# Kernel tuning notes

Measured on AMD Instinct MI355X. Metric: run time of the kernel, lower is better.

The kernel has to match this reference:

```python
import jax, jax.numpy as jnp
import numpy as np
import math

NUM_HEADS = 8
EMBED = 512
D_K = EMBED // NUM_HEADS
B, T1, T2 = 16, 512, 512
N_POS = 2 * T1 - 1


def rel_shift(x, left_context=0):
    # x: (B, H, T1, 2*T1-1) -> (B, H, T1, T2), out[i, j] = x[i, j - i + T1 - 1]
    t1 = x.shape[2]
    t2 = t1 + left_context
    idx = jnp.arange(t2)[None, :] - jnp.arange(t1)[:, None] + (t1 - 1)  # (T1, T2)
    return jnp.take_along_axis(x, idx[None, None, :, :], axis=-1)


def setup_inputs() -> dict:
    key = jax.random.key(0)
    ks = jax.random.split(key, 16)
    scale = 1.0 / math.sqrt(EMBED)
    inp = {
        "query": jax.random.normal(ks[0], (B, T1, EMBED), jnp.float32),
        "key": jax.random.normal(ks[1], (B, T2, EMBED), jnp.float32),
        "value": jax.random.normal(ks[2], (B, T2, EMBED), jnp.float32),
        "pos_enc": jax.random.normal(ks[3], (B, N_POS, EMBED), jnp.float32),
        "mask": jnp.zeros((B, T2), dtype=bool),
        "chunk_mask": jnp.zeros((T1, T1), dtype=bool),
        "Wq": jax.random.normal(ks[4], (EMBED, EMBED), jnp.float32) * scale,
        "bq": jnp.zeros((EMBED,), jnp.float32),
        "Wk": jax.random.normal(ks[5], (EMBED, EMBED), jnp.float32) * scale,
        "bk": jnp.zeros((EMBED,), jnp.float32),
        "Wv": jax.random.normal(ks[6], (EMBED, EMBED), jnp.float32) * scale,
        "bv": jnp.zeros((EMBED,), jnp.float32),
        "Wpos": jax.random.normal(ks[7], (EMBED, EMBED), jnp.float32) * scale,
        "Wo": jax.random.normal(ks[8], (EMBED, EMBED), jnp.float32) * scale,
        "bo": jnp.zeros((EMBED,), jnp.float32),
        "pos_bias_u": jax.random.normal(ks[9], (NUM_HEADS, D_K), jnp.float32) * 0.1,
        "pos_bias_v": jax.random.normal(ks[10], (NUM_HEADS, D_K), jnp.float32) * 0.1,
        "left_context": 0,
    }
    return inp


def reference(query, key, value, pos_enc, mask, chunk_mask, Wq, bq, Wk, bk, Wv, bv,
              Wpos, Wo, bo, pos_bias_u, pos_bias_v, left_context):
    b, t1, _ = query.shape
    t2 = key.shape[1]
    # qkv projections -> (B, T, H, d_k)
    q = (query @ Wq.T + bq).reshape(b, t1, NUM_HEADS, D_K)
    k = (key @ Wk.T + bk).reshape(b, t2, NUM_HEADS, D_K)
    v = (value @ Wv.T + bv).reshape(b, t2, NUM_HEADS, D_K)
    # positional projection (no bias) -> (B, N, H, d_k)
    p = (pos_enc @ Wpos.T).reshape(b, -1, NUM_HEADS, D_K)
    # content and positional scores
    matrix_ac = jnp.einsum('bihd,bjhd->bhij', q + pos_bias_u, k)  # (B,H,T1,T2)
    matrix_bd = jnp.einsum('bihd,bnhd->bhin', q + pos_bias_v, p)  # (B,H,T1,N)
    matrix_bd = rel_shift(matrix_bd, left_context=left_context)   # (B,H,T1,T2)
    scores = (matrix_ac + matrix_bd) / math.sqrt(D_K)
    # combined mask: True = masked
    m = chunk_mask[None, None, :, :] | mask[:, None, None, :]
    neg_inf = jnp.finfo(scores.dtype).min
    scores = jnp.where(m, neg_inf, scores)
    attn = jax.nn.softmax(scores, axis=-1)
    attn = jnp.where(m, 0.0, attn)
    out = jnp.einsum('bhij,bjhd->bihd', attn, v).reshape(b, t1, NUM_HEADS * D_K)
    return out @ Wo.T + bo
```

## Files before the change

kernel.cpp:

```cpp
#include <hip/hip_runtime.h>
#include <math.h>

typedef _Float16 f16;
typedef f16 f16x8 __attribute__((ext_vector_type(8)));
typedef f16 f16x4 __attribute__((ext_vector_type(4)));
typedef float f32x4 __attribute__((ext_vector_type(4)));

#define H_   8
#define E_   512
#define DK   64
#define BB   16
#define T1C  512
#define T2C  512
#define NPOS 1023

__device__ __forceinline__ f16x8 cvt8(const float4 a, const float4 b) {
    f16x8 h;
    h[0] = (f16)a.x; h[1] = (f16)a.y; h[2] = (f16)a.z; h[3] = (f16)a.w;
    h[4] = (f16)b.x; h[5] = (f16)b.y; h[6] = (f16)b.z; h[7] = (f16)b.w;
    return h;
}

struct PArg {
    const void* A; const float* W; const float* bias; const float* bias2;
    void* C; int Mvalid; int mode; int a16;
};
struct PArgs { PArg g[4]; };

__device__ __forceinline__ void gemm64_body(const PArg g, int bx, int by) {
    __shared__ f16 Al[64 * 40];
    __shared__ f16 Wl[64 * 40];
    const int tid = threadIdx.x;
    const int lane = tid & 63, w = tid >> 6;
    const int quad = lane >> 4, l15 = lane & 15;
    const int m0 = by * 64, n0 = bx * 64;
    const int row = tid >> 2, koff = (tid & 3) * 8;
    int arow = m0 + row; if (arow >= g.Mvalid) arow = g.Mvalid - 1;
    const size_t aoff = (size_t)arow * 512 + koff;
    const size_t woff = (size_t)(n0 + row) * 512 + koff;

    f32x4 acc[4];
    #pragma unroll
    for (int nt = 0; nt < 4; ++nt) acc[nt] = (f32x4){0.f, 0.f, 0.f, 0.f};

    float4 fa0, fa1, fw0, fw1;
    uint4 ha;
    if (g.a16) {
        ha = *(const uint4*)((const f16*)g.A + aoff);
    } else {
        fa0 = *(const float4*)((const float*)g.A + aoff);
        fa1 = *(const float4*)((const float*)g.A + aoff + 4);
    }
    fw0 = *(const float4*)(g.W + woff);
    fw1 = *(const float4*)(g.W + woff + 4);

    for (int ki = 0; ki < 16; ++ki) {
        __syncthreads();
        if (g.a16) *(uint4*)&Al[row * 40 + koff] = ha;
        else       *(f16x8*)&Al[row * 40 + koff] = cvt8(fa0, fa1);
        *(f16x8*)&Wl[row * 40 + koff] = cvt8(fw0, fw1);
        __syncthreads();
        if (ki < 15) {
            const int k0 = (ki + 1) * 32;
            if (g.a16) {
                ha = *(const uint4*)((const f16*)g.A + aoff + k0);
            } else {
                fa0 = *(const float4*)((const float*)g.A + aoff + k0);
                fa1 = *(const float4*)((const float*)g.A + aoff + k0 + 4);
            }
            fw0 = *(const float4*)(g.W + woff + k0);
            fw1 = *(const float4*)(g.W + woff + k0 + 4);
        }
        const f16x8 af = *(const f16x8*)&Al[(w * 16 + l15) * 40 + quad * 8];
        #pragma unroll
        for (int nt = 0; nt < 4; ++nt) {
            const f16x8 bf = *(const f16x8*)&Wl[(nt * 16 + l15) * 40 + quad * 8];
            acc[nt] = __builtin_amdgcn_mfma_f32_16x16x32_f16(af, bf, acc[nt], 0, 0, 0);
        }
    }

    const int mb = m0 + w * 16 + quad * 4;
    #pragma unroll
    for (int nt = 0; nt < 4; ++nt) {
        const int n = n0 + nt * 16 + l15;
        const f32x4 a = acc[nt];
        float bs = g.bias ? g.bias[n] : 0.f;
        if (g.bias2) bs += g.bias2[n];
        if (g.mode == 0) {
            float* C = (float*)g.C;
            #pragma unroll
            for (int r = 0; r < 4; ++r) C[(size_t)(mb + r) * 512 + n] = a[r] + bs;
        } else if (g.mode == 1) {
            f16* C = (f16*)g.C;
            const int b = mb >> 9, t = mb & 511;
            const int hh = n >> 6, dk = n & 63;
            f16x4 h;
            #pragma unroll
            for (int r = 0; r < 4; ++r) h[r] = (f16)(a[r] + bs);
            *(f16x4*)&C[(((size_t)b * H_ + hh) * DK + dk) * 512 + t] = h;
        } else if (g.mode == 2) {
            f16* C = (f16*)g.C;
            const int b = mb >> 9, t = mb & 511;
            const int hh = n >> 6, dk = n & 63;
            #pragma unroll
            for (int r = 0; r < 4; ++r)
                C[(((size_t)b * H_ + hh) * 512 + t + r) * DK + dk] = (f16)(a[r] + bs);
        } else {
            f16* C = (f16*)g.C;
            const int hh = n >> 6, dk = n & 63;
            #pragma unroll
            for (int r = 0; r < 4; ++r) {
                const int m = mb + r;
                if (m < g.Mvalid) {
                    const int b = m / NPOS, t = m - b * NPOS;
                    C[(((size_t)b * H_ + hh) * NPOS + t) * DK + dk] = (f16)a[r];
                }
            }
        }
    }
}

__device__ __forceinline__ int xcd_swz(int rem, int nwg) {
    return (rem & 7) * (nwg >> 3) + (rem >> 3);
}

__global__ __launch_bounds__(256) void proj_all(PArgs a) {
    const int id = blockIdx.x;
    int gi, rem, nwg;
    if (id < 3072) { gi = id >> 10; rem = id & 1023; nwg = 1024; }
    else           { gi = 3;        rem = id - 3072; nwg = 2048; }
    const int t = xcd_swz(rem, nwg);
    gemm64_body(a.g[gi], t & 7, t >> 3);
}
__global__ __launch_bounds__(256) void proj_one(PArg g) {
    const int t = xcd_swz(blockIdx.x, 1024);
    gemm64_body(g, t & 7, t >> 3);
}

__global__ __launch_bounds__(256) void attn_mfma(
    const f16* __restrict__ Qh,
    const f16* __restrict__ Kh,
    const f16* __restrict__ Vt,
    const f16* __restrict__ Ph,
    const float* __restrict__ pbu, const float* __restrict__ pbv,
    const unsigned char* __restrict__ bmask,
    const unsigned char* __restrict__ cmask,
    f16* __restrict__ CTX)
{
    __shared__ f16 Qa[64 * 72];
    __shared__ f16 Ka[64 * 72];
    __shared__ f16 Va[64 * 72];
    __shared__ f16 Pa[128 * 72];
    __shared__ unsigned char Ma[64 * 64];

    const int tid = threadIdx.x;
    const int lane = tid & 63, w = tid >> 6;
    const int quad = lane >> 4, l15 = lane & 15;
    const int id = blockIdx.x;
    const int lg = (id & 7) * 128 + (id >> 3);
    const int it = lg & 7, bh = lg >> 3;
    const int h = bh & 7, b = bh >> 3;
    const int i0 = it * 64;
    const int rowt = w * 16 + quad * 4;
    const int sr = tid >> 3, sc = (tid & 7) * 8;
    const int mr = tid >> 2, mc = (tid & 3) * 16;

    *(uint4*)&Qa[sr * 72 + sc] = *(const uint4*)&Qh[((size_t)bh * 512 + i0 + sr) * 64 + sc];
    *(uint4*)&Qa[(sr + 32) * 72 + sc] =
        *(const uint4*)&Qh[((size_t)bh * 512 + i0 + sr + 32) * 64 + sc];
    f16x8 dpbf[2];
    #pragma unroll
    for (int ks = 0; ks < 2; ++ks)
        #pragma unroll
        for (int j = 0; j < 8; ++j) {
            const int d = ks * 32 + quad * 8 + j;
            dpbf[ks][j] = (f16)(pbv[h * 64 + d] - pbu[h * 64 + d]);
        }

    float m_run[4], l_run[4];
    f32x4 accO[4];
    #pragma unroll
    for (int x = 0; x < 4; ++x) {
        m_run[x] = -__builtin_inff(); l_run[x] = 0.f;
        accO[x] = (f32x4){0.f, 0.f, 0.f, 0.f};
    }

    uint4 pK0, pK1, pV0, pV1, pP0, pP1, pP2, pP3, pM;
    {
        const int j0 = 0, nbase = 448 - i0;
        pK0 = *(const uint4*)&Kh[((size_t)bh * 512 + j0 + sr) * 64 + sc];
        pK1 = *(const uint4*)&Kh[((size_t)bh * 512 + j0 + sr + 32) * 64 + sc];
        pV0 = *(const uint4*)&Vt[((size_t)bh * 64 + sr) * 512 + j0 + sc];
        pV1 = *(const uint4*)&Vt[((size_t)bh * 64 + sr + 32) * 512 + j0 + sc];
        int n0_ = nbase + sr;       if (n0_ > NPOS - 1) n0_ = NPOS - 1;
        int n1_ = nbase + sr + 32;  if (n1_ > NPOS - 1) n1_ = NPOS - 1;
        int n2_ = nbase + sr + 64;  if (n2_ > NPOS - 1) n2_ = NPOS - 1;
        int n3_ = nbase + sr + 96;  if (n3_ > NPOS - 1) n3_ = NPOS - 1;
        pP0 = *(const uint4*)&Ph[((size_t)bh * NPOS + n0_) * 64 + sc];
        pP1 = *(const uint4*)&Ph[((size_t)bh * NPOS + n1_) * 64 + sc];
        pP2 = *(const uint4*)&Ph[((size_t)bh * NPOS + n2_) * 64 + sc];
        pP3 = *(const uint4*)&Ph[((size_t)bh * NPOS + n3_) * 64 + sc];
        const uint4 cm = *(const uint4*)&cmask[(size_t)(i0 + mr) * 512 + j0 + mc];
        const uint4 bm = *(const uint4*)&bmask[(size_t)b * 512 + j0 + mc];
        pM.x = cm.x | bm.x; pM.y = cm.y | bm.y; pM.z = cm.z | bm.z; pM.w = cm.w | bm.w;
    }

    for (int jt = 0; jt < 8; ++jt) {
        __syncthreads();
        *(uint4*)&Ka[sr * 72 + sc] = pK0;
        *(uint4*)&Ka[(sr + 32) * 72 + sc] = pK1;
        *(uint4*)&Va[sr * 72 + sc] = pV0;
        *(uint4*)&Va[(sr + 32) * 72 + sc] = pV1;
        *(uint4*)&Pa[sr * 72 + sc] = pP0;
        *(uint4*)&Pa[(sr + 32) * 72 + sc] = pP1;
        *(uint4*)&Pa[(sr + 64) * 72 + sc] = pP2;
        *(uint4*)&Pa[(sr + 96) * 72 + sc] = pP3;
        *(uint4*)&Ma[mr * 64 + mc] = pM;
        __syncthreads();

        if (jt < 7) {
            const int j0n = (jt + 1) * 64;
            const int nbase = j0n - i0 + 448;
            pK0 = *(const uint4*)&Kh[((size_t)bh * 512 + j0n + sr) * 64 + sc];
            pK1 = *(const uint4*)&Kh[((size_t)bh * 512 + j0n + sr + 32) * 64 + sc];
            pV0 = *(const uint4*)&Vt[((size_t)bh * 64 + sr) * 512 + j0n + sc];
            pV1 = *(const uint4*)&Vt[((size_t)bh * 64 + sr + 32) * 512 + j0n + sc];
            int n0_ = nbase + sr;       if (n0_ > NPOS - 1) n0_ = NPOS - 1;
            int n1_ = nbase + sr + 32;  if (n1_ > NPOS - 1) n1_ = NPOS - 1;
            int n2_ = nbase + sr + 64;  if (n2_ > NPOS - 1) n2_ = NPOS - 1;
            int n3_ = nbase + sr + 96;  if (n3_ > NPOS - 1) n3_ = NPOS - 1;
            pP0 = *(const uint4*)&Ph[((size_t)bh * NPOS + n0_) * 64 + sc];
            pP1 = *(const uint4*)&Ph[((size_t)bh * NPOS + n1_) * 64 + sc];
            pP2 = *(const uint4*)&Ph[((size_t)bh * NPOS + n2_) * 64 + sc];
            pP3 = *(const uint4*)&Ph[((size_t)bh * NPOS + n3_) * 64 + sc];
            const uint4 cm = *(const uint4*)&cmask[(size_t)(i0 + mr) * 512 + j0n + mc];
            const uint4 bm = *(const uint4*)&bmask[(size_t)b * 512 + j0n + mc];
            pM.x = cm.x | bm.x; pM.y = cm.y | bm.y; pM.z = cm.z | bm.z; pM.w = cm.w | bm.w;
        }

        f16x8 afQ[2], afV[2];
        #pragma unroll
        for (int ks = 0; ks < 2; ++ks) {
            afQ[ks] = *(const f16x8*)&Qa[(w * 16 + l15) * 72 + ks * 32 + quad * 8];
            afV[ks] = afQ[ks] + dpbf[ks];
        }
        f32x4 accAC[4];
        #pragma unroll
        for (int nt = 0; nt < 4; ++nt) {
            accAC[nt] = (f32x4){0.f, 0.f, 0.f, 0.f};
            #pragma unroll
            for (int ks = 0; ks < 2; ++ks) {
                const f16x8 bf = *(const f16x8*)&Ka[(nt * 16 + l15) * 72 + ks * 32 + quad * 8];
                accAC[nt] = __builtin_amdgcn_mfma_f32_16x16x32_f16(afQ[ks], bf, accAC[nt], 0, 0, 0);
            }
        }
        f32x4 accBD[5];
        #pragma unroll
        for (int u = 0; u < 5; ++u) {
            accBD[u] = (f32x4){0.f, 0.f, 0.f, 0.f};
            const int nts = (3 - w) + u;
            #pragma unroll
            for (int ks = 0; ks < 2; ++ks) {
                const f16x8 bf = *(const f16x8*)&Pa[(nts * 16 + l15) * 72 + ks * 32 + quad * 8];
                accBD[u] = __builtin_amdgcn_mfma_f32_16x16x32_f16(afV[ks], bf, accBD[u], 0, 0, 0);
            }
        }
        __syncthreads();

        #pragma unroll
        for (int rg = 0; rg < 4; ++rg) {
            const int qr = quad * 4 + rg;
            const int rt = rowt + rg;
            float tmpv[5];
            #pragma unroll
            for (int u = 0; u < 5; ++u) {
                const int cl = l15 + (3 + u) * 16 + qr - 63;
                const int dst = (quad * 16 + (cl & 15)) << 2;
                tmpv[u] = __uint_as_float(
                    (unsigned)__builtin_amdgcn_ds_permute(dst, (int)__float_as_uint(accBD[u][rg])));
            }
            const bool hi = l15 > qr;
            float sv[4]; unsigned mk = 0;
            #pragma unroll
            for (int nt = 0; nt < 4; ++nt) {
                const int c = nt * 16 + l15;
                const float bdv = hi ? tmpv[nt + 1] : tmpv[nt];
                float s = (accAC[nt][rg] + bdv) * 0.125f;
                if (Ma[rt * 64 + c]) { s = -3.402823466e38f; mk |= 1u << nt; }
                sv[nt] = s;
            }
            float tmax = fmaxf(fmaxf(sv[0], sv[1]), fmaxf(sv[2], sv[3]));
            #pragma unroll
            for (int d = 1; d < 16; d <<= 1) tmax = fmaxf(tmax, __shfl_xor(tmax, d));
            const float mnew = fmaxf(m_run[rg], tmax);
            const float alpha = __expf(m_run[rg] - mnew);
            float rsum = 0.f;
            f16 wv[4];
            #pragma unroll
            for (int nt = 0; nt < 4; ++nt) {
                const float e = __expf(sv[nt] - mnew);
                rsum += e;
                wv[nt] = ((mk >> nt) & 1u) ? (f16)0.f : (f16)e;
            }
            #pragma unroll
            for (int d = 1; d < 16; d <<= 1) rsum += __shfl_xor(rsum, d);
            l_run[rg] = l_run[rg] * alpha + rsum;
            m_run[rg] = mnew;
            #pragma unroll
            for (int dt = 0; dt < 4; ++dt) accO[dt][rg] *= alpha;
            #pragma unroll
            for (int nt = 0; nt < 4; ++nt)
                Ka[rt * 72 + nt * 16 + l15] = wv[nt];
        }
        f16x8 afW[2];
        #pragma unroll
        for (int ks = 0; ks < 2; ++ks)
            afW[ks] = *(const f16x8*)&Ka[(w * 16 + l15) * 72 + ks * 32 + quad * 8];
        #pragma unroll
        for (int dt = 0; dt < 4; ++dt)
            #pragma unroll
            for (int ks = 0; ks < 2; ++ks) {
                const f16x8 bf = *(const f16x8*)&Va[(dt * 16 + l15) * 72 + ks * 32 + quad * 8];
                accO[dt] = __builtin_amdgcn_mfma_f32_16x16x32_f16(afW[ks], bf, accO[dt], 0, 0, 0);
            }
    }

    #pragma unroll
    for (int rg = 0; rg < 4; ++rg) {
        const float inv = 1.0f / l_run[rg];
        const int gi = i0 + rowt + rg;
        #pragma unroll
        for (int dt = 0; dt < 4; ++dt)
            CTX[((size_t)b * 512 + gi) * 512 + h * 64 + dt * 16 + l15] = (f16)(accO[dt][rg] * inv);
    }
}

extern "C" void kernel_launch(void* const* d_in, const int* in_sizes, int n_in,
                              void* d_out, int out_size, void* d_ws, size_t ws_size,
                              hipStream_t stream) {
    const float* query   = (const float*)d_in[0];
    const float* key     = (const float*)d_in[1];
    const float* value   = (const float*)d_in[2];
    const float* pos_enc = (const float*)d_in[3];
    const unsigned char* mask       = (const unsigned char*)d_in[4];
    const unsigned char* chunk_mask = (const unsigned char*)d_in[5];
    const float* Wq  = (const float*)d_in[6];
    const float* bq  = (const float*)d_in[7];
    const float* Wk  = (const float*)d_in[8];
    const float* bk  = (const float*)d_in[9];
    const float* Wv  = (const float*)d_in[10];
    const float* bv  = (const float*)d_in[11];
    const float* Wpos = (const float*)d_in[12];
    const float* Wo   = (const float*)d_in[13];
    const float* bo   = (const float*)d_in[14];
    const float* pbu  = (const float*)d_in[15];
    const float* pbv  = (const float*)d_in[16];
    float* out = (float*)d_out;

    f16* base = (f16*)d_ws;
    size_t off = 0;
    f16* ctx = base + off; off += 4194304;
    f16* Qhm = base + off; off += 4194304;
    f16* Khm = base + off; off += 4194304;
    f16* Vtm = base + off; off += 4194304;
    f16* Phm = base + off; off += 8380416;

    PArgs pa;
    pa.g[0] = PArg{query,   Wq,   bq, pbu,     (void*)Qhm, 8192,  2, 0};
    pa.g[1] = PArg{key,     Wk,   bk, nullptr, (void*)Khm, 8192,  2, 0};
    pa.g[2] = PArg{value,   Wv,   bv, nullptr, (void*)Vtm, 8192,  1, 0};
    pa.g[3] = PArg{pos_enc, Wpos, nullptr, nullptr, (void*)Phm, 16368, 3, 0};
    proj_all<<<dim3(5120), 256, 0, stream>>>(pa);

    attn_mfma<<<dim3(1024), 256, 0, stream>>>(Qhm, Khm, Vtm, Phm, pbu, pbv,
                                              mask, chunk_mask, ctx);

    PArg go = PArg{ctx, Wo, bo, nullptr, (void*)out, 8192, 0, 1};
    proj_one<<<dim3(1024), 256, 0, stream>>>(go);
}
```

Before: 295.0 us.

## Enlarge projection GEMM tiles to 128x128 with double-buffered swizzled LDS

```diff
diff --git a/kernel.cpp b/kernel.cpp
--- a/kernel.cpp
+++ b/kernel.cpp
@@ -9,9 +9,6 @@
 #define H_   8
 #define E_   512
 #define DK   64
-#define BB   16
-#define T1C  512
-#define T2C  512
 #define NPOS 1023
 
 __device__ __forceinline__ f16x8 cvt8(const float4 a, const float4 b) {
@@ -27,114 +24,132 @@
 };
 struct PArgs { PArg g[4]; };
 
-__device__ __forceinline__ void gemm64_body(const PArg g, int bx, int by) {
-    __shared__ f16 Al[64 * 40];
-    __shared__ f16 Wl[64 * 40];
+__device__ __forceinline__ void gemm128_body(const PArg g, int bx, int by) {
+    __shared__ __align__(16) f16 Al[2][128 * 32];
+    __shared__ __align__(16) f16 Wl[2][128 * 32];
     const int tid = threadIdx.x;
     const int lane = tid & 63, w = tid >> 6;
     const int quad = lane >> 4, l15 = lane & 15;
-    const int m0 = by * 64, n0 = bx * 64;
-    const int row = tid >> 2, koff = (tid & 3) * 8;
-    int arow = m0 + row; if (arow >= g.Mvalid) arow = g.Mvalid - 1;
-    const size_t aoff = (size_t)arow * 512 + koff;
-    const size_t woff = (size_t)(n0 + row) * 512 + koff;
-
-    f32x4 acc[4];
-    #pragma unroll
-    for (int nt = 0; nt < 4; ++nt) acc[nt] = (f32x4){0.f, 0.f, 0.f, 0.f};
-
-    float4 fa0, fa1, fw0, fw1;
-    uint4 ha;
-    if (g.a16) {
-        ha = *(const uint4*)((const f16*)g.A + aoff);
-    } else {
-        fa0 = *(const float4*)((const float*)g.A + aoff);
-        fa1 = *(const float4*)((const float*)g.A + aoff + 4);
-    }
-    fw0 = *(const float4*)(g.W + woff);
-    fw1 = *(const float4*)(g.W + woff + 4);
-
+    const int wr = w >> 1, wc = w & 1;
+    const int m0 = by * 128, n0 = bx * 128;
+    const int srow = tid >> 1, half = tid & 1;
+    int arow = m0 + srow; if (arow >= g.Mvalid) arow = g.Mvalid - 1;
+    const size_t aoff = (size_t)arow * 512 + half * 16;
+    const size_t woff = (size_t)(n0 + srow) * 512 + half * 16;
+    const int swr = (srow ^ (srow >> 2)) & 3;
+    const int wo0 = srow * 32 + (((half * 2)     ^ swr) * 8);
+    const int wo1 = srow * 32 + (((half * 2 + 1) ^ swr) * 8);
+    const int swl = (l15 ^ (l15 >> 2)) & 3;
+    const int rch = (quad ^ swl) * 8;
+
+    f32x4 acc[4][4];
+    #pragma unroll
+    for (int m = 0; m < 4; ++m)
+        #pragma unroll
+        for (int n = 0; n < 4; ++n) acc[m][n] = (f32x4){0.f, 0.f, 0.f, 0.f};
+
+    float4 fa0, fa1, fa2, fa3, fw0, fw1, fw2, fw3;
+    uint4 ha0, ha1;
+
+    #define LOADA(K0) do { \
+        if (g.a16) { const f16* Ah = (const f16*)g.A + aoff + (K0); \
+                     ha0 = *(const uint4*)Ah; ha1 = *(const uint4*)(Ah + 8); } \
+        else { const float* Af = (const float*)g.A + aoff + (K0); \
+               fa0 = *(const float4*)Af;       fa1 = *(const float4*)(Af + 4); \
+               fa2 = *(const float4*)(Af + 8); fa3 = *(const float4*)(Af + 12); } } while (0)
+    #define LOADW(K0) do { const float* Wf = g.W + woff + (K0); \
+        fw0 = *(const float4*)Wf;        fw1 = *(const float4*)(Wf + 4); \
+        fw2 = *(const float4*)(Wf + 8);  fw3 = *(const float4*)(Wf + 12); } while (0)
+    #define STAGE(buf) do { \
+        if (g.a16) { *(uint4*)&Al[buf][wo0] = ha0; *(uint4*)&Al[buf][wo1] = ha1; } \
+        else { *(f16x8*)&Al[buf][wo0] = cvt8(fa0, fa1); *(f16x8*)&Al[buf][wo1] = cvt8(fa2, fa3); } \
+        *(f16x8*)&Wl[buf][wo0] = cvt8(fw0, fw1); *(f16x8*)&Wl[buf][wo1] = cvt8(fw2, fw3); } while (0)
+
+    LOADA(0); LOADW(0);
+    STAGE(0);
+    LOADA(32); LOADW(32);
+    __syncthreads();
+
+    #pragma unroll 2
     for (int ki = 0; ki < 16; ++ki) {
+        const int cur = ki & 1, nxt = cur ^ 1;
+        if (ki < 15) STAGE(nxt);
+        if (ki < 14) { LOADA((ki + 2) * 32); LOADW((ki + 2) * 32); }
+        f16x8 af[4], bf[4];
+        #pragma unroll
+        for (int m = 0; m < 4; ++m)
+            af[m] = *(const f16x8*)&Al[cur][(wr * 64 + m * 16 + l15) * 32 + rch];
+        #pragma unroll
+        for (int n = 0; n < 4; ++n)
+            bf[n] = *(const f16x8*)&Wl[cur][(wc * 64 + n * 16 + l15) * 32 + rch];
+        #pragma unroll
+        for (int m = 0; m < 4; ++m)
+            #pragma unroll
+            for (int n = 0; n < 4; ++n)
+                acc[m][n] = __builtin_amdgcn_mfma_f32_16x16x32_f16(af[m], bf[n], acc[m][n], 0, 0, 0);
         __syncthreads();
-        if (g.a16) *(uint4*)&Al[row * 40 + koff] = ha;
-        else       *(f16x8*)&Al[row * 40 + koff] = cvt8(fa0, fa1);
-        *(f16x8*)&Wl[row * 40 + koff] = cvt8(fw0, fw1);
-        __syncthreads();
-        if (ki < 15) {
-            const int k0 = (ki + 1) * 32;
-            if (g.a16) {
-                ha = *(const uint4*)((const f16*)g.A + aoff + k0);
+    }
+    #undef LOADA
+    #undef LOADW
+    #undef STAGE
+
+    const int mq = m0 + wr * 64 + quad * 4;
+    const int nq = n0 + wc * 64 + l15;
+    #pragma unroll
+    for (int m = 0; m < 4; ++m) {
+        #pragma unroll
+        for (int n = 0; n < 4; ++n) {
+            const int gr0 = mq + m * 16;
+            const int col = nq + n * 16;
+            float bs = g.bias ? g.bias[col] : 0.f;
+            if (g.bias2) bs += g.bias2[col];
+            const f32x4 a = acc[m][n];
+            if (g.mode == 0) {
+                float* C = (float*)g.C;
+                #pragma unroll
+                for (int r = 0; r < 4; ++r) C[(size_t)(gr0 + r) * 512 + col] = a[r] + bs;
+            } else if (g.mode == 1) {
+                f16* C = (f16*)g.C;
+                const int b = gr0 >> 9, t = gr0 & 511;
+                const int hh = col >> 6, dk = col & 63;
+                f16x4 hv;
+                #pragma unroll
+                for (int r = 0; r < 4; ++r) hv[r] = (f16)(a[r] + bs);
+                *(f16x4*)&C[(((size_t)b * H_ + hh) * DK + dk) * 512 + t] = hv;
+            } else if (g.mode == 2) {
+                f16* C = (f16*)g.C;
+                const int b = gr0 >> 9, t = gr0 & 511;
+                const int hh = col >> 6, dk = col & 63;
+                #pragma unroll
+                for (int r = 0; r < 4; ++r)
+                    C[(((size_t)b * H_ + hh) * 512 + t + r) * DK + dk] = (f16)(a[r] + bs);
             } else {
-                fa0 = *(const float4*)((const float*)g.A + aoff + k0);
-                fa1 = *(const float4*)((const float*)g.A + aoff + k0 + 4);
-            }
-            fw0 = *(const float4*)(g.W + woff + k0);
-            fw1 = *(const float4*)(g.W + woff + k0 + 4);
-        }
-        const f16x8 af = *(const f16x8*)&Al[(w * 16 + l15) * 40 + quad * 8];
-        #pragma unroll
-        for (int nt = 0; nt < 4; ++nt) {
-            const f16x8 bf = *(const f16x8*)&Wl[(nt * 16 + l15) * 40 + quad * 8];
-            acc[nt] = __builtin_amdgcn_mfma_f32_16x16x32_f16(af, bf, acc[nt], 0, 0, 0);
-        }
-    }
-
-    const int mb = m0 + w * 16 + quad * 4;
-    #pragma unroll
-    for (int nt = 0; nt < 4; ++nt) {
-        const int n = n0 + nt * 16 + l15;
-        const f32x4 a = acc[nt];
-        float bs = g.bias ? g.bias[n] : 0.f;
-        if (g.bias2) bs += g.bias2[n];
-        if (g.mode == 0) {
-            float* C = (float*)g.C;
-            #pragma unroll
-            for (int r = 0; r < 4; ++r) C[(size_t)(mb + r) * 512 + n] = a[r] + bs;
-        } else if (g.mode == 1) {
-            f16* C = (f16*)g.C;
-            const int b = mb >> 9, t = mb & 511;
-            const int hh = n >> 6, dk = n & 63;
-            f16x4 h;
-            #pragma unroll
-            for (int r = 0; r < 4; ++r) h[r] = (f16)(a[r] + bs);
-            *(f16x4*)&C[(((size_t)b * H_ + hh) * DK + dk) * 512 + t] = h;
-        } else if (g.mode == 2) {
-            f16* C = (f16*)g.C;
-            const int b = mb >> 9, t = mb & 511;
-            const int hh = n >> 6, dk = n & 63;
-            #pragma unroll
-            for (int r = 0; r < 4; ++r)
-                C[(((size_t)b * H_ + hh) * 512 + t + r) * DK + dk] = (f16)(a[r] + bs);
-        } else {
-            f16* C = (f16*)g.C;
-            const int hh = n >> 6, dk = n & 63;
-            #pragma unroll
-            for (int r = 0; r < 4; ++r) {
-                const int m = mb + r;
-                if (m < g.Mvalid) {
-                    const int b = m / NPOS, t = m - b * NPOS;
-                    C[(((size_t)b * H_ + hh) * NPOS + t) * DK + dk] = (f16)a[r];
+                f16* C = (f16*)g.C;
+                const int hh = col >> 6, dk = col & 63;
+                #pragma unroll
+                for (int r = 0; r < 4; ++r) {
+                    const int gm = gr0 + r;
+                    if (gm < g.Mvalid) {
+                        const int b = gm / NPOS, t = gm - b * NPOS;
+                        C[(((size_t)b * H_ + hh) * NPOS + t) * DK + dk] = (f16)a[r];
+                    }
                 }
             }
         }
     }
 }
 
-__device__ __forceinline__ int xcd_swz(int rem, int nwg) {
-    return (rem & 7) * (nwg >> 3) + (rem >> 3);
-}
-
-__global__ __launch_bounds__(256) void proj_all(PArgs a) {
+__global__ __launch_bounds__(256, 3) void proj_all(PArgs a) {
     const int id = blockIdx.x;
     int gi, rem, nwg;
-    if (id < 3072) { gi = id >> 10; rem = id & 1023; nwg = 1024; }
-    else           { gi = 3;        rem = id - 3072; nwg = 2048; }
-    const int t = xcd_swz(rem, nwg);
-    gemm64_body(a.g[gi], t & 7, t >> 3);
-}
-__global__ __launch_bounds__(256) void proj_one(PArg g) {
-    const int t = xcd_swz(blockIdx.x, 1024);
-    gemm64_body(g, t & 7, t >> 3);
+    if (id < 768) { gi = id >> 8; rem = id & 255; nwg = 256; }
+    else          { gi = 3;       rem = id - 768; nwg = 512; }
+    const int t = (rem & 7) * (nwg >> 3) + (rem >> 3);
+    gemm128_body(a.g[gi], t & 3, t >> 2);
+}
+__global__ __launch_bounds__(256, 3) void proj_one(PArg g) {
+    const int t = (blockIdx.x & 7) * 32 + (blockIdx.x >> 3);
+    gemm128_body(g, t & 3, t >> 2);
 }
 
 __global__ __launch_bounds__(256) void attn_mfma(
@@ -370,11 +385,11 @@
     pa.g[1] = PArg{key,     Wk,   bk, nullptr, (void*)Khm, 8192,  2, 0};
     pa.g[2] = PArg{value,   Wv,   bv, nullptr, (void*)Vtm, 8192,  1, 0};
     pa.g[3] = PArg{pos_enc, Wpos, nullptr, nullptr, (void*)Phm, 16368, 3, 0};
-    proj_all<<<dim3(5120), 256, 0, stream>>>(pa);
+    proj_all<<<dim3(1280), 256, 0, stream>>>(pa);
 
     attn_mfma<<<dim3(1024), 256, 0, stream>>>(Qhm, Khm, Vtm, Phm, pbu, pbv,
                                               mask, chunk_mask, ctx);
 
     PArg go = PArg{ctx, Wo, bo, nullptr, (void*)out, 8192, 0, 1};
-    proj_one<<<dim3(1024), 256, 0, stream>>>(go);
-}
+    proj_one<<<dim3(256), 256, 0, stream>>>(go);
+}
```

Result: faster. 287.6 us (-2.5%).
